# Kernel tuning notes

Hardware: AMD Instinct MI355X
Metric: run time of the kernel (lower is better)

The kernel has to match this reference:

```python
import jax, jax.numpy as jnp
import numpy as np
from jax import lax

B_, L_ = 2, 512
D_MODEL, EXPAND, HEAD_DIM, NGROUPS, D_STATE, D_CONV = 512, 2, 64, 1, 64, 3
D_INNER = EXPAND * D_MODEL            # 1024
NHEADS = D_INNER // HEAD_DIM          # 16
CONV_DIM = D_INNER + 2 * NGROUPS * D_STATE   # 1152
D_IN_PROJ = 2 * D_INNER + 2 * NGROUPS * D_STATE + NHEADS  # 2192
RMS_EPS = 1e-5


def silu(x):
    return x * jax.nn.sigmoid(x)


def segsum(x):
    # x: (..., T) -> (..., T, T); out[..., i, j] = sum_{j<k<=i} x[..., k], -inf above diag
    T = x.shape[-1]
    xr = jnp.broadcast_to(x[..., None], x.shape + (T,))
    keep = jnp.tril(jnp.ones((T, T), dtype=bool), -1)
    xr = jnp.where(keep, xr, 0.0)
    s = jnp.cumsum(xr, axis=-2)
    diag = jnp.tril(jnp.ones((T, T), dtype=bool), 0)
    return jnp.where(diag, s, -jnp.inf)


def ssd(x, A, Bm, Cm, chunk):
    # x: (b,l,h,p), A: (b,l,h), Bm/Cm: (b,l,g,n); chunk==1 as in the source forward
    b, l, h, p = x.shape
    c = l // chunk
    n = Bm.shape[-1]
    x = x.reshape(b, c, chunk, h, p)
    Bm = Bm.reshape(b, c, chunk, Bm.shape[2], n)
    Cm = Cm.reshape(b, c, chunk, Cm.shape[2], n)
    A = A.reshape(b, c, chunk, h).transpose(0, 3, 1, 2)        # (b,h,c,l)
    A_cumsum = jnp.cumsum(A, axis=-1)
    Lmat = jnp.exp(segsum(A))                                   # (b,h,c,l,l)
    # broadcast group dim (g==1) to heads, matching torch.einsum broadcasting
    Bb = jnp.broadcast_to(Bm, (b, c, chunk, h, n))
    Cb = jnp.broadcast_to(Cm, (b, c, chunk, h, n))
    Y_diag = jnp.einsum('bclhn,bcshn,bhcls,bcshp->bclhp', Cb, Bb, Lmat, x)
    decay_states = jnp.exp(A_cumsum[:, :, :, -1:] - A_cumsum)   # (b,h,c,l)
    states = jnp.einsum('bclhn,bhcl,bclhp->bchpn', Bb, decay_states, x)
    states = jnp.concatenate([jnp.zeros_like(states[:, :1]), states], axis=1)  # (b,c+1,h,p,n)
    A_last = jnp.pad(A_cumsum[:, :, :, -1], ((0, 0), (0, 0), (1, 0)))          # (b,h,c+1)
    decay_chunk = jnp.exp(segsum(A_last))                       # (b,h,c+1,c+1)
    new_states = jnp.einsum('bhzc,bchpn->bzhpn', decay_chunk, states)
    states = new_states[:, :-1]                                 # (b,c,h,p,n)
    state_decay_out = jnp.exp(A_cumsum)
    Y_off = jnp.einsum('bclhn,bchpn,bhcl->bclhp', Cb, states, state_decay_out)
    return (Y_diag + Y_off).reshape(b, l, h, p)


def causal_dwconv(x, w, bias):
    # x: (B,L,C); w: (C,K) depthwise; torch pads (K-1) both sides then slices [:L] == left-pad only
    xt = x.transpose(0, 2, 1)
    y = lax.conv_general_dilated(xt, w[:, None, :], (1,), [(D_CONV - 1, 0)],
                                 feature_group_count=CONV_DIM,
                                 dimension_numbers=('NCH', 'OIH', 'NCH'))
    return y.transpose(0, 2, 1) + bias


def setup_inputs() -> dict:
    key = jax.random.key(0)
    ks = jax.random.split(key, 8)
    u = jax.random.normal(ks[0], (B_, L_, D_MODEL), dtype=jnp.float32)
    W_in = jax.random.normal(ks[1], (D_MODEL, D_IN_PROJ), dtype=jnp.float32) / np.sqrt(D_MODEL).astype(np.float32)
    conv_w = jax.random.normal(ks[2], (CONV_DIM, D_CONV), dtype=jnp.float32) * 0.3
    conv_b = jnp.zeros((CONV_DIM,), dtype=jnp.float32)
    dt = jnp.exp(jax.random.uniform(ks[3], (NHEADS,), dtype=jnp.float32)
                 * (np.float32(np.log(0.1)) - np.float32(np.log(0.001))) + np.float32(np.log(0.001)))
    dt = jnp.clip(dt, 1e-4, None)
    dt_bias = dt + jnp.log(-jnp.expm1(-dt))
    A_log = jnp.log(jax.random.uniform(ks[4], (NHEADS,), dtype=jnp.float32, minval=1.0, maxval=16.0))
    D_param = jnp.ones((NHEADS,), dtype=jnp.float32)
    rms_w = jnp.ones((D_INNER,), dtype=jnp.float32)
    W_out = jax.random.normal(ks[5], (D_INNER, D_MODEL), dtype=jnp.float32) / np.sqrt(D_INNER).astype(np.float32)
    return {"u": u, "W_in": W_in, "conv_w": conv_w, "conv_b": conv_b, "dt_bias": dt_bias,
            "A_log": A_log, "D_param": D_param, "rms_w": rms_w, "W_out": W_out}


def reference(u, W_in, conv_w, conv_b, dt_bias, A_log, D_param, rms_w, W_out):
    b, l, _ = u.shape
    zxbcdt = u @ W_in                                   # (b,l,D_IN_PROJ)
    z = zxbcdt[..., :D_INNER]
    xBC = zxbcdt[..., D_INNER:D_INNER + CONV_DIM]
    dt = zxbcdt[..., D_INNER + CONV_DIM:]
    dt = jax.nn.softplus(dt + dt_bias)                  # (b,l,h)
    A = -jnp.exp(A_log)                                 # (h,)
    xBC = silu(causal_dwconv(xBC, conv_w, conv_b))      # (b,l,CONV_DIM)
    x = xBC[..., :D_INNER].reshape(b, l, NHEADS, HEAD_DIM)
    Bm = xBC[..., D_INNER:D_INNER + D_STATE][:, :, None, :]     # (b,l,1,n)
    Cm = xBC[..., D_INNER + D_STATE:][:, :, None, :]            # (b,l,1,n)
    y = ssd(x * dt[..., None], A * dt, Bm, Cm, 1)       # (b,l,h,p)
    y = y + x * D_param[:, None]
    y = y.reshape(b, l, D_INNER)
    # gated RMSNorm
    yz = y * silu(z)
    y = yz * lax.rsqrt(jnp.mean(yz * yz, axis=-1, keepdims=True) + RMS_EPS) * rms_w
    return y @ W_out
```

## Files before the change

### kernel.cpp

```cpp
#include <hip/hip_runtime.h>
#include <hip/hip_bf16.h>

#define B_SZ 2
#define L_SZ 512
#define D_MODEL 512
#define D_INNER 1024
#define HEAD_DIM 64
#define NHEADS 16
#define D_STATE 64
#define D_CONV 3
#define CONV_DIM 1152
#define D_IN_PROJ 2192
#define BL (B_SZ * L_SZ)
#define RMS_EPS 1e-5f
#define QC 64
#define NCH 8
#define NPAD1 2304
#define PB 72

typedef __attribute__((ext_vector_type(8))) short short8t;
typedef __attribute__((ext_vector_type(8))) unsigned short ushort8t;
typedef __attribute__((ext_vector_type(4))) unsigned short ushort4t;
typedef __attribute__((ext_vector_type(4))) float f32x4;

__device__ __forceinline__ unsigned short f2bf(float f) {
    unsigned u = __float_as_uint(f);
    u += 0x7fff + ((u >> 16) & 1);
    return (unsigned short)(u >> 16);
}
__device__ __forceinline__ float bf2f(unsigned short u) {
    return __uint_as_float(((unsigned)u) << 16);
}

__device__ __forceinline__ void gload_lds16(const void* g, void* lds) {
    __builtin_amdgcn_global_load_lds(
        (const __attribute__((address_space(1))) unsigned int*)g,
        (__attribute__((address_space(3))) unsigned int*)lds, 16, 0, 0);
}

__device__ __forceinline__ void transpose_tile_bf16(const float* __restrict__ src,
                                                    unsigned short* __restrict__ dst,
                                                    int K, int Nin, int tile, int ntn) {
    __shared__ float T[64][65];
    int tid = threadIdx.x;
    int nt = tile % ntn, kt = tile / ntn;
    int n0 = nt * 64, k0 = kt * 64;
#pragma unroll
    for (int rr = 0; rr < 4; ++rr) {
        int k = k0 + (tid >> 4) + rr * 16;
        int nn = (tid & 15) * 4;
#pragma unroll
        for (int q = 0; q < 4; ++q) {
            int n = n0 + nn + q;
            T[(tid >> 4) + rr * 16][nn + q] = (n < Nin) ? src[(size_t)k * Nin + n] : 0.f;
        }
    }
    __syncthreads();
    int nn2 = tid >> 2, kc = tid & 3;
    unsigned short ov[16];
#pragma unroll
    for (int j = 0; j < 16; ++j) ov[j] = f2bf(T[kc * 16 + j][nn2]);
    unsigned short* p = dst + (size_t)(n0 + nn2) * K + k0 + kc * 16;
    *(ushort8t*)p = *(ushort8t*)&ov[0];
    *(ushort8t*)(p + 8) = *(ushort8t*)&ov[8];
}

__global__ __launch_bounds__(256) void prep_kernel(const float* __restrict__ W_in,
                                                   const float* __restrict__ W_out,
                                                   const float* __restrict__ u,
                                                   unsigned short* __restrict__ Wt1,
                                                   unsigned short* __restrict__ Wt2,
                                                   unsigned short* __restrict__ u_bf) {
    int bid = blockIdx.x;
    if (bid < 288) {
        transpose_tile_bf16(W_in, Wt1, D_MODEL, D_IN_PROJ, bid, 36);
    } else if (bid < 416) {
        transpose_tile_bf16(W_out, Wt2, D_INNER, D_MODEL, bid - 288, 8);
    } else {
        int i = ((bid - 416) * 256 + threadIdx.x) * 8;
        float4 v0 = *(const float4*)(u + i);
        float4 v1 = *(const float4*)(u + i + 4);
        unsigned short ov[8] = {f2bf(v0.x), f2bf(v0.y), f2bf(v0.z), f2bf(v0.w),
                                f2bf(v1.x), f2bf(v1.y), f2bf(v1.z), f2bf(v1.w)};
        *(ushort8t*)(u_bf + i) = *(ushort8t*)&ov[0];
    }
}

__global__ __launch_bounds__(256) void gemm_mfma64(const unsigned short* __restrict__ A,
                                                   const unsigned short* __restrict__ Bt,
                                                   float* __restrict__ C,
                                                   int N, int K) {
    __shared__ char sm[49152];
    int tid = threadIdx.x;
    int w = tid >> 6, l = tid & 63;
    int m0 = blockIdx.y * 64, n0 = blockIdx.x * 64;
    int wm = w >> 1, wn = w & 1;

    f32x4 acc[2][2];
#pragma unroll
    for (int i = 0; i < 2; ++i)
#pragma unroll
        for (int j = 0; j < 2; ++j) acc[i][j] = (f32x4){0.f, 0.f, 0.f, 0.f};

    auto stage = [&](const unsigned short* src, int row0, int k0, char* dst) {
#pragma unroll
        for (int p = 0; p < 2; ++p) {
            int c = w * 2 + p;
            int row = c * 8 + (l >> 3);
            int scb = ((l & 7) << 4) ^ ((row & 7) << 4);
            gload_lds16(src + (size_t)(row0 + row) * K + k0 + (scb >> 1), dst + c * 1024);
        }
    };

    int nkt = K / 64;
    stage(A, m0, 0, sm);
    stage(Bt, n0, 0, sm + 8192);
    if (nkt > 1) {
        stage(A, m0, 64, sm + 16384);
        stage(Bt, n0, 64, sm + 16384 + 8192);
    }

    for (int kt = 0; kt < nkt; ++kt) {
        if (kt + 2 < nkt) {
            char* d = sm + ((kt + 2) % 3) * 16384;
            stage(A, m0, (kt + 2) * 64, d);
            stage(Bt, n0, (kt + 2) * 64, d + 8192);
        }
        int inflight = nkt - 1 - kt;
        if (inflight >= 2)      asm volatile("s_waitcnt vmcnt(8)" ::: "memory");
        else if (inflight == 1) asm volatile("s_waitcnt vmcnt(4)" ::: "memory");
        else                    asm volatile("s_waitcnt vmcnt(0)" ::: "memory");
        __builtin_amdgcn_s_barrier();

        const char* Ab = sm + (kt % 3) * 16384;
        const char* Bb = Ab + 8192;
#pragma unroll
        for (int kk = 0; kk < 2; ++kk) {
            short8t af[2], bf[2];
#pragma unroll
            for (int i = 0; i < 2; ++i) {
                int r = wm * 32 + i * 16 + (l & 15);
                int cb = (kk * 64 + (l >> 4) * 16) ^ ((r & 7) << 4);
                af[i] = *(const short8t*)(Ab + r * 128 + cb);
            }
#pragma unroll
            for (int j = 0; j < 2; ++j) {
                int r = wn * 32 + j * 16 + (l & 15);
                int cb = (kk * 64 + (l >> 4) * 16) ^ ((r & 7) << 4);
                bf[j] = *(const short8t*)(Bb + r * 128 + cb);
            }
#pragma unroll
            for (int i = 0; i < 2; ++i)
#pragma unroll
                for (int j = 0; j < 2; ++j)
                    acc[i][j] = __builtin_amdgcn_mfma_f32_16x16x32_bf16(af[i], bf[j], acc[i][j], 0, 0, 0);
        }
        __builtin_amdgcn_s_barrier();
    }

#pragma unroll
    for (int i = 0; i < 2; ++i)
#pragma unroll
        for (int j = 0; j < 2; ++j) {
            int row = m0 + wm * 32 + i * 16 + (l >> 4) * 4;
            int col = n0 + wn * 32 + j * 16 + (l & 15);
            if (col < N) {
#pragma unroll
                for (int r = 0; r < 4; ++r)
                    C[(size_t)(row + r) * N + col] = acc[i][j][r];
            }
        }
}

__device__ __forceinline__ float4 conv4(const float* __restrict__ prow, int gl, int zxcol,
                                        const float* __restrict__ conv_w,
                                        const float* __restrict__ conv_b) {
    float4 v2 = *(const float4*)(prow + zxcol);
    float4 v1 = make_float4(0.f, 0.f, 0.f, 0.f), v0 = v1;
    if (gl >= 1) v1 = *(const float4*)(prow - D_IN_PROJ + zxcol);
    if (gl >= 2) v0 = *(const float4*)(prow - 2 * D_IN_PROJ + zxcol);
    int ch = zxcol - D_INNER;
    float4 o;
    float a;
    a = conv_b[ch+0] + conv_w[(ch+0)*3]*v0.x + conv_w[(ch+0)*3+1]*v1.x + conv_w[(ch+0)*3+2]*v2.x;
    o.x = a / (1.f + __expf(-a));
    a = conv_b[ch+1] + conv_w[(ch+1)*3]*v0.y + conv_w[(ch+1)*3+1]*v1.y + conv_w[(ch+1)*3+2]*v2.y;
    o.y = a / (1.f + __expf(-a));
    a = conv_b[ch+2] + conv_w[(ch+2)*3]*v0.z + conv_w[(ch+2)*3+1]*v1.z + conv_w[(ch+2)*3+2]*v2.z;
    o.z = a / (1.f + __expf(-a));
    a = conv_b[ch+3] + conv_w[(ch+3)*3]*v0.w + conv_w[(ch+3)*3+1]*v1.w + conv_w[(ch+3)*3+2]*v2.w;
    o.w = a / (1.f + __expf(-a));
    return o;
}

__global__ __launch_bounds__(256) void ssd_passA(const float* __restrict__ zxbcdt,
                                                 const float* __restrict__ conv_w,
                                                 const float* __restrict__ conv_b,
                                                 const float* __restrict__ dt_bias,
                                                 const float* __restrict__ A_log,
                                                 const float* __restrict__ D_param,
                                                 float* __restrict__ y,
                                                 float* __restrict__ Zbuf,
                                                 float* __restrict__ Ebuf) {
    int blk = blockIdx.x;
    int h = blk & 15;
    int c = (blk >> 4) & 7;
    int b = blk >> 7;
    int tid = threadIdx.x;

    __shared__ __align__(16) unsigned short Cs_bf[QC][PB];
    __shared__ __align__(16) unsigned short Bs_bf[QC][PB];
    __shared__ __align__(16) unsigned short BT_bf[QC][PB];
    __shared__ __align__(16) unsigned short XDT_bf[QC][PB];
    __shared__ __align__(16) unsigned short XDTw_bf[QC][PB];
    __shared__ __align__(16) unsigned short P_bf[QC][PB];
    __shared__ float csh[QC], dts[QC], wh[QC];

    int bl0 = b * L_SZ + c * QC;
    const float* zb = zxbcdt + (size_t)bl0 * D_IN_PROJ;

    if (tid < 64) {
        int t = tid;
        float draw = zb[(size_t)t * D_IN_PROJ + 2 * D_INNER + 2 * D_STATE + h];
        float dtv = draw + dt_bias[h];
        dtv = (dtv > 20.f) ? dtv : log1pf(expf(dtv));
        float A = -expf(A_log[h]);
        float cs = A * dtv;
#pragma unroll
        for (int off = 1; off < 64; off <<= 1) {
            float tmp = __shfl_up(cs, off);
            if (t >= off) cs += tmp;
        }
        float cs63 = __shfl(cs, 63);
        dts[t] = dtv;
        csh[t] = cs;
        wh[t] = __expf(cs63 - cs);
        Ebuf[(((size_t)(b * NHEADS + h) * NCH) + c) * QC + t] = __expf(cs);
    }

    int row16 = tid >> 4;
    int col4 = (tid & 15) * 4;
#pragma unroll
    for (int r = 0; r < 4; ++r) {
        int t = r * 16 + row16;
        int gl = c * QC + t;
        const float* prow = zb + (size_t)t * D_IN_PROJ;
        float4 Bv = conv4(prow, gl, D_INNER + D_INNER + col4, conv_w, conv_b);
        float4 Cv = conv4(prow, gl, D_INNER + D_INNER + D_STATE + col4, conv_w, conv_b);
        ushort4t bq = {f2bf(Bv.x), f2bf(Bv.y), f2bf(Bv.z), f2bf(Bv.w)};
        ushort4t cq = {f2bf(Cv.x), f2bf(Cv.y), f2bf(Cv.z), f2bf(Cv.w)};
        *(ushort4t*)&Bs_bf[t][col4] = bq;
        *(ushort4t*)&Cs_bf[t][col4] = cq;
#pragma unroll
        for (int q = 0; q < 4; ++q) BT_bf[col4 + q][t] = bq[q];
    }
    __syncthreads();

#pragma unroll
    for (int r = 0; r < 4; ++r) {
        int t = r * 16 + row16;
        int gl = c * QC + t;
        const float* prow = zb + (size_t)t * D_IN_PROJ;
        float4 xv = conv4(prow, gl, D_INNER + h * HEAD_DIM + col4, conv_w, conv_b);
        float d = dts[t], wt = wh[t];
        xv.x *= d; xv.y *= d; xv.z *= d; xv.w *= d;
        ushort4t xq = {f2bf(xv.x), f2bf(xv.y), f2bf(xv.z), f2bf(xv.w)};
        ushort4t xwq = {f2bf(xv.x * wt), f2bf(xv.y * wt), f2bf(xv.z * wt), f2bf(xv.w * wt)};
#pragma unroll
        for (int q = 0; q < 4; ++q) {
            XDT_bf[col4 + q][t] = xq[q];
            XDTw_bf[col4 + q][t] = xwq[q];
        }
    }

    int l = tid & 63, wv = tid >> 6;
    int wm = wv >> 1, wn = wv & 1;
    int fr = l & 15, fq = l >> 4;

    {
        f32x4 g[2][2];
#pragma unroll
        for (int i = 0; i < 2; ++i)
#pragma unroll
            for (int j = 0; j < 2; ++j) g[i][j] = (f32x4){0.f, 0.f, 0.f, 0.f};
#pragma unroll
        for (int kk = 0; kk < 2; ++kk) {
            short8t af[2], bb[2];
#pragma unroll
            for (int i = 0; i < 2; ++i)
                af[i] = *(const short8t*)&Cs_bf[wm * 32 + i * 16 + fr][kk * 32 + fq * 8];
#pragma unroll
            for (int j = 0; j < 2; ++j)
                bb[j] = *(const short8t*)&Bs_bf[wn * 32 + j * 16 + fr][kk * 32 + fq * 8];
#pragma unroll
            for (int i = 0; i < 2; ++i)
#pragma unroll
                for (int j = 0; j < 2; ++j)
                    g[i][j] = __builtin_amdgcn_mfma_f32_16x16x32_bf16(af[i], bb[j], g[i][j], 0, 0, 0);
        }
#pragma unroll
        for (int i = 0; i < 2; ++i)
#pragma unroll
            for (int j = 0; j < 2; ++j) {
                int s = wn * 32 + j * 16 + fr;
                float css = csh[s];
#pragma unroll
                for (int r = 0; r < 4; ++r) {
                    int t = wm * 32 + i * 16 + fq * 4 + r;
                    float v = (s <= t) ? g[i][j][r] * __expf(csh[t] - css) : 0.f;
                    P_bf[t][s] = f2bf(v);
                }
            }
    }
    __syncthreads();

    {
        f32x4 yv[2][2];
#pragma unroll
        for (int i = 0; i < 2; ++i)
#pragma unroll
            for (int j = 0; j < 2; ++j) yv[i][j] = (f32x4){0.f, 0.f, 0.f, 0.f};
#pragma unroll
        for (int kk = 0; kk < 2; ++kk) {
            short8t af[2], bb[2];
#pragma unroll
            for (int i = 0; i < 2; ++i)
                af[i] = *(const short8t*)&P_bf[wm * 32 + i * 16 + fr][kk * 32 + fq * 8];
#pragma unroll
            for (int j = 0; j < 2; ++j)
                bb[j] = *(const short8t*)&XDT_bf[wn * 32 + j * 16 + fr][kk * 32 + fq * 8];
#pragma unroll
            for (int i = 0; i < 2; ++i)
#pragma unroll
                for (int j = 0; j < 2; ++j)
                    yv[i][j] = __builtin_amdgcn_mfma_f32_16x16x32_bf16(af[i], bb[j], yv[i][j], 0, 0, 0);
        }
        float Dp = D_param[h];
#pragma unroll
        for (int i = 0; i < 2; ++i)
#pragma unroll
            for (int j = 0; j < 2; ++j) {
                int p = wn * 32 + j * 16 + fr;
#pragma unroll
                for (int r = 0; r < 4; ++r) {
                    int t = wm * 32 + i * 16 + fq * 4 + r;
                    float xval = bf2f(XDT_bf[p][t]);
                    float fct = Dp / dts[t];
                    y[(size_t)(bl0 + t) * D_INNER + h * HEAD_DIM + p] =
                        yv[i][j][r] + fct * xval;
                }
            }
    }

    {
        f32x4 zv[2][2];
#pragma unroll
        for (int i = 0; i < 2; ++i)
#pragma unroll
            for (int j = 0; j < 2; ++j) zv[i][j] = (f32x4){0.f, 0.f, 0.f, 0.f};
#pragma unroll
        for (int kk = 0; kk < 2; ++kk) {
            short8t af[2], bb[2];
#pragma unroll
            for (int i = 0; i < 2; ++i)
                af[i] = *(const short8t*)&XDTw_bf[wm * 32 + i * 16 + fr][kk * 32 + fq * 8];
#pragma unroll
            for (int j = 0; j < 2; ++j)
                bb[j] = *(const short8t*)&BT_bf[wn * 32 + j * 16 + fr][kk * 32 + fq * 8];
#pragma unroll
            for (int i = 0; i < 2; ++i)
#pragma unroll
                for (int j = 0; j < 2; ++j)
                    zv[i][j] = __builtin_amdgcn_mfma_f32_16x16x32_bf16(af[i], bb[j], zv[i][j], 0, 0, 0);
        }
        float* Zr = Zbuf + (((size_t)(b * NHEADS + h) * NCH) + c) * (HEAD_DIM * D_STATE);
#pragma unroll
        for (int i = 0; i < 2; ++i)
#pragma unroll
            for (int j = 0; j < 2; ++j) {
                int n = wn * 32 + j * 16 + fr;
#pragma unroll
                for (int r = 0; r < 4; ++r) {
                    int p = wm * 32 + i * 16 + fq * 4 + r;
                    Zr[p * D_STATE + n] = zv[i][j][r];
                }
            }
    }
}

__global__ __launch_bounds__(256) void ssd_passC(const float* __restrict__ zxbcdt,
                                                 const float* __restrict__ conv_w,
                                                 const float* __restrict__ conv_b,
                                                 const float* __restrict__ Zbuf,
                                                 const float* __restrict__ Ebuf,
                                                 float* __restrict__ y) {
    int blk = blockIdx.x;
    int h = blk & 15;
    int c = (blk >> 4) & 7;
    int b = blk >> 7;
    if (c == 0) return;
    int tid = threadIdx.x;

    __shared__ __align__(16) unsigned short Cs_bf[QC][PB];
    __shared__ __align__(16) unsigned short S_bf[QC][PB];
    __shared__ float Eh[QC];

    int bl0 = b * L_SZ + c * QC;
    const float* zb = zxbcdt + (size_t)bl0 * D_IN_PROJ;
    const float* Zb = Zbuf + ((size_t)(b * NHEADS + h) * NCH) * (HEAD_DIM * D_STATE);
    const float* Eb = Ebuf + ((size_t)(b * NHEADS + h) * NCH) * QC;

    {
        int p = tid >> 2, nq = (tid & 3) * 16;
        float S16[16];
#pragma unroll
        for (int q = 0; q < 16; ++q) S16[q] = 0.f;
        float wgt = 1.f;
        for (int j = c - 1; j >= 0; --j) {
            const float* Zj = Zb + (size_t)j * (HEAD_DIM * D_STATE) + p * D_STATE + nq;
#pragma unroll
            for (int q4 = 0; q4 < 4; ++q4) {
                float4 z = *(const float4*)(Zj + q4 * 4);
                S16[q4 * 4 + 0] += wgt * z.x;
                S16[q4 * 4 + 1] += wgt * z.y;
                S16[q4 * 4 + 2] += wgt * z.z;
                S16[q4 * 4 + 3] += wgt * z.w;
            }
            wgt *= Eb[(size_t)j * QC + 63];
        }
#pragma unroll
        for (int q4 = 0; q4 < 4; ++q4) {
            ushort4t s4 = {f2bf(S16[q4 * 4 + 0]), f2bf(S16[q4 * 4 + 1]),
                           f2bf(S16[q4 * 4 + 2]), f2bf(S16[q4 * 4 + 3])};
            *(ushort4t*)&S_bf[p][nq + q4 * 4] = s4;
        }
    }

    int row16 = tid >> 4, col4 = (tid & 15) * 4;
#pragma unroll
    for (int r = 0; r < 4; ++r) {
        int t = r * 16 + row16;
        int gl = c * QC + t;
        float4 Cv = conv4(zb + (size_t)t * D_IN_PROJ, gl,
                          D_INNER + D_INNER + D_STATE + col4, conv_w, conv_b);
        ushort4t cq = {f2bf(Cv.x), f2bf(Cv.y), f2bf(Cv.z), f2bf(Cv.w)};
        *(ushort4t*)&Cs_bf[t][col4] = cq;
    }
    if (tid < 64)
        Eh[tid] = Ebuf[(((size_t)(b * NHEADS + h) * NCH) + c) * QC + tid];
    __syncthreads();

    int l = tid & 63, wv = tid >> 6;
    int wm = wv >> 1, wn = wv & 1;
    int fr = l & 15, fq = l >> 4;
    f32x4 acc[2][2];
#pragma unroll
    for (int i = 0; i < 2; ++i)
#pragma unroll
        for (int j = 0; j < 2; ++j) acc[i][j] = (f32x4){0.f, 0.f, 0.f, 0.f};
#pragma unroll
    for (int kk = 0; kk < 2; ++kk) {
        short8t af[2], bb[2];
#pragma unroll
        for (int i = 0; i < 2; ++i)
            af[i] = *(const short8t*)&Cs_bf[wm * 32 + i * 16 + fr][kk * 32 + fq * 8];
#pragma unroll
        for (int j = 0; j < 2; ++j)
            bb[j] = *(const short8t*)&S_bf[wn * 32 + j * 16 + fr][kk * 32 + fq * 8];
#pragma unroll
        for (int i = 0; i < 2; ++i)
#pragma unroll
            for (int j = 0; j < 2; ++j)
                acc[i][j] = __builtin_amdgcn_mfma_f32_16x16x32_bf16(af[i], bb[j], acc[i][j], 0, 0, 0);
    }
#pragma unroll
    for (int i = 0; i < 2; ++i)
#pragma unroll
        for (int j = 0; j < 2; ++j) {
            int p = wn * 32 + j * 16 + fr;
#pragma unroll
            for (int r = 0; r < 4; ++r) {
                int t = wm * 32 + i * 16 + fq * 4 + r;
                float* yp = y + (size_t)(bl0 + t) * D_INNER + h * HEAD_DIM + p;
                *yp += Eh[t] * acc[i][j][r];
            }
        }
}

__global__ __launch_bounds__(256) void gated_rmsnorm_kernel(const float* __restrict__ zxbcdt,
                                                            const float* __restrict__ y,
                                                            const float* __restrict__ rms_w,
                                                            unsigned short* __restrict__ yn_bf) {
    int bl = blockIdx.x;
    int tid = threadIdx.x;
    __shared__ float red[4];
    __shared__ float sscale;
    float vals[4];
    float sumsq = 0.f;
#pragma unroll
    for (int i = 0; i < 4; ++i) {
        int col = tid + i * 256;
        float yv = y[(size_t)bl * D_INNER + col];
        float z = zxbcdt[(size_t)bl * D_IN_PROJ + col];
        float yz = yv * (z / (1.f + expf(-z)));
        vals[i] = yz;
        sumsq += yz * yz;
    }
#pragma unroll
    for (int off = 32; off; off >>= 1) sumsq += __shfl_xor(sumsq, off);
    int wave = tid >> 6, lane = tid & 63;
    if (lane == 0) red[wave] = sumsq;
    __syncthreads();
    if (tid == 0) {
        float t = red[0] + red[1] + red[2] + red[3];
        sscale = rsqrtf(t / (float)D_INNER + RMS_EPS);
    }
    __syncthreads();
    float sc = sscale;
#pragma unroll
    for (int i = 0; i < 4; ++i) {
        int col = tid + i * 256;
        yn_bf[(size_t)bl * D_INNER + col] = f2bf(vals[i] * sc * rms_w[col]);
    }
}

extern "C" void kernel_launch(void* const* d_in, const int* in_sizes, int n_in,
                              void* d_out, int out_size, void* d_ws, size_t ws_size,
                              hipStream_t stream) {
    const float* u       = (const float*)d_in[0];
    const float* W_in    = (const float*)d_in[1];
    const float* conv_w  = (const float*)d_in[2];
    const float* conv_b  = (const float*)d_in[3];
    const float* dt_bias = (const float*)d_in[4];
    const float* A_log   = (const float*)d_in[5];
    const float* D_param = (const float*)d_in[6];
    const float* rms_w   = (const float*)d_in[7];
    const float* W_out   = (const float*)d_in[8];
    float* out = (float*)d_out;

    float* ws = (float*)d_ws;
    float* zxbcdt = ws;
    float* y      = zxbcdt + (size_t)BL * D_IN_PROJ;
    float* Zbuf   = y + (size_t)BL * D_INNER;
    float* Ebuf   = Zbuf + (size_t)32 * NCH * 4096;
    unsigned short* u_bf  = (unsigned short*)(Ebuf + 32 * NCH * QC);
    unsigned short* Wt1   = u_bf + (size_t)BL * D_MODEL;
    unsigned short* Wt2   = Wt1 + (size_t)NPAD1 * D_MODEL;
    unsigned short* yn_bf = Wt2 + (size_t)D_MODEL * D_INNER;

    prep_kernel<<<672, 256, 0, stream>>>(W_in, W_out, u, Wt1, Wt2, u_bf);

    gemm_mfma64<<<dim3(NPAD1 / 64, BL / 64), 256, 0, stream>>>(
        u_bf, Wt1, zxbcdt, D_IN_PROJ, D_MODEL);

    ssd_passA<<<B_SZ * NCH * NHEADS, 256, 0, stream>>>(
        zxbcdt, conv_w, conv_b, dt_bias, A_log, D_param, y, Zbuf, Ebuf);
    ssd_passC<<<B_SZ * NCH * NHEADS, 256, 0, stream>>>(
        zxbcdt, conv_w, conv_b, Zbuf, Ebuf, y);

    gated_rmsnorm_kernel<<<BL, 256, 0, stream>>>(zxbcdt, y, rms_w, yn_bf);

    gemm_mfma64<<<dim3(D_MODEL / 64, BL / 64), 256, 0, stream>>>(
        yn_bf, Wt2, out, D_MODEL, D_INNER);
}
```

Before: 47.46 us.

## Fuse gated RMSNorm into output GEMM and fold rms weight into W_out

Removes the separate gated RMSNorm kernel and its bf16 intermediate. The output GEMM now loads y and z, applies the SiLU gate and converts to bf16 as it stages A tiles, and accumulates per-row sums of squares so the rsqrt scale is applied in the epilogue. rms_w is folded into the transposed W_out during prep, and passC no longer launches idle blocks for chunk 0. This saves one launch and a full round trip through memory. The cost is that each of the 8 column blocks recomputes the gate and row norms, and the GEMM uses smaller 32-row tiles.

```diff
diff --git a/kernel.cpp b/kernel.cpp
--- a/kernel.cpp
+++ b/kernel.cpp
@@ -39,6 +39,7 @@
 }
 
 __device__ __forceinline__ void transpose_tile_bf16(const float* __restrict__ src,
+                                                    const float* __restrict__ scale,
                                                     unsigned short* __restrict__ dst,
                                                     int K, int Nin, int tile, int ntn) {
     __shared__ float T[64][65];
@@ -48,11 +49,12 @@
 #pragma unroll
     for (int rr = 0; rr < 4; ++rr) {
         int k = k0 + (tid >> 4) + rr * 16;
+        float sc = scale ? scale[k] : 1.f;
         int nn = (tid & 15) * 4;
 #pragma unroll
         for (int q = 0; q < 4; ++q) {
             int n = n0 + nn + q;
-            T[(tid >> 4) + rr * 16][nn + q] = (n < Nin) ? src[(size_t)k * Nin + n] : 0.f;
+            T[(tid >> 4) + rr * 16][nn + q] = (n < Nin) ? src[(size_t)k * Nin + n] * sc : 0.f;
         }
     }
     __syncthreads();
@@ -67,15 +69,16 @@
 
 __global__ __launch_bounds__(256) void prep_kernel(const float* __restrict__ W_in,
                                                    const float* __restrict__ W_out,
+                                                   const float* __restrict__ rms_w,
                                                    const float* __restrict__ u,
                                                    unsigned short* __restrict__ Wt1,
                                                    unsigned short* __restrict__ Wt2,
                                                    unsigned short* __restrict__ u_bf) {
     int bid = blockIdx.x;
     if (bid < 288) {
-        transpose_tile_bf16(W_in, Wt1, D_MODEL, D_IN_PROJ, bid, 36);
+        transpose_tile_bf16(W_in, nullptr, Wt1, D_MODEL, D_IN_PROJ, bid, 36);
     } else if (bid < 416) {
-        transpose_tile_bf16(W_out, Wt2, D_INNER, D_MODEL, bid - 288, 8);
+        transpose_tile_bf16(W_out, rms_w, Wt2, D_INNER, D_MODEL, bid - 288, 8);
     } else {
         int i = ((bid - 416) * 256 + threadIdx.x) * 8;
         float4 v0 = *(const float4*)(u + i);
@@ -396,9 +399,9 @@
                                                  float* __restrict__ y) {
     int blk = blockIdx.x;
     int h = blk & 15;
-    int c = (blk >> 4) & 7;
-    int b = blk >> 7;
-    if (c == 0) return;
+    int q = blk >> 4;
+    int c = 1 + (q % 7);
+    int b = q / 7;
     int tid = threadIdx.x;
 
     __shared__ __align__(16) unsigned short Cs_bf[QC][PB];
@@ -414,7 +417,7 @@
         int p = tid >> 2, nq = (tid & 3) * 16;
         float S16[16];
 #pragma unroll
-        for (int q = 0; q < 16; ++q) S16[q] = 0.f;
+        for (int qq = 0; qq < 16; ++qq) S16[qq] = 0.f;
         float wgt = 1.f;
         for (int j = c - 1; j >= 0; --j) {
             const float* Zj = Zb + (size_t)j * (HEAD_DIM * D_STATE) + p * D_STATE + nq;
@@ -487,40 +490,117 @@
         }
 }
 
-__global__ __launch_bounds__(256) void gated_rmsnorm_kernel(const float* __restrict__ zxbcdt,
-                                                            const float* __restrict__ y,
-                                                            const float* __restrict__ rms_w,
-                                                            unsigned short* __restrict__ yn_bf) {
-    int bl = blockIdx.x;
+__global__ __launch_bounds__(256) void gemm_out_fused(const float* __restrict__ y,
+                                                      const float* __restrict__ zxbcdt,
+                                                      const unsigned short* __restrict__ Bt,
+                                                      float* __restrict__ out) {
+    __shared__ char sm[2][12288];
+    __shared__ float red[32][8];
+    __shared__ float srow[32];
     int tid = threadIdx.x;
-    __shared__ float red[4];
-    __shared__ float sscale;
-    float vals[4];
+    int w = tid >> 6, l = tid & 63;
+    int m0 = blockIdx.y * 32, n0 = blockIdx.x * 64;
+    int wm = w >> 1, wn = w & 1;
+
+    f32x4 acc[2];
+    acc[0] = (f32x4){0.f, 0.f, 0.f, 0.f};
+    acc[1] = (f32x4){0.f, 0.f, 0.f, 0.f};
+
+    int ar = tid >> 3, ac8 = tid & 7;
+    const float* yrow = y + (size_t)(m0 + ar) * D_INNER + ac8 * 8;
+    const float* zrow = zxbcdt + (size_t)(m0 + ar) * D_IN_PROJ + ac8 * 8;
     float sumsq = 0.f;
-#pragma unroll
-    for (int i = 0; i < 4; ++i) {
-        int col = tid + i * 256;
-        float yv = y[(size_t)bl * D_INNER + col];
-        float z = zxbcdt[(size_t)bl * D_IN_PROJ + col];
-        float yz = yv * (z / (1.f + expf(-z)));
-        vals[i] = yz;
-        sumsq += yz * yz;
-    }
-#pragma unroll
-    for (int off = 32; off; off >>= 1) sumsq += __shfl_xor(sumsq, off);
-    int wave = tid >> 6, lane = tid & 63;
-    if (lane == 0) red[wave] = sumsq;
+
+    auto stageB = [&](int k0, char* dstB) {
+#pragma unroll
+        for (int p = 0; p < 2; ++p) {
+            int cc = w * 2 + p;
+            int row = cc * 8 + (l >> 3);
+            int scb = ((l & 7) << 4) ^ ((row & 7) << 4);
+            gload_lds16(Bt + (size_t)(n0 + row) * D_INNER + k0 + (scb >> 1), dstB + cc * 1024);
+        }
+    };
+
+    float4 vy0, vy1, vz0, vz1;
+    auto loadA = [&](int k0) {
+        vy0 = *(const float4*)(yrow + k0);
+        vy1 = *(const float4*)(yrow + k0 + 4);
+        vz0 = *(const float4*)(zrow + k0);
+        vz1 = *(const float4*)(zrow + k0 + 4);
+    };
+    auto writeA = [&](char* dstA) {
+        float yv[8] = {vy0.x, vy0.y, vy0.z, vy0.w, vy1.x, vy1.y, vy1.z, vy1.w};
+        float zv[8] = {vz0.x, vz0.y, vz0.z, vz0.w, vz1.x, vz1.y, vz1.z, vz1.w};
+        unsigned short o[8];
+#pragma unroll
+        for (int qq = 0; qq < 8; ++qq) {
+            float vv = yv[qq] * (zv[qq] / (1.f + __expf(-zv[qq])));
+            sumsq += vv * vv;
+            o[qq] = f2bf(vv);
+        }
+        int b0 = ac8 * 16;
+        *(ushort8t*)(dstA + ar * 128 + (b0 ^ ((ar & 7) << 4))) = *(ushort8t*)o;
+    };
+
+    loadA(0);
+    stageB(0, sm[0] + 4096);
+    writeA(sm[0]);
+    asm volatile("s_waitcnt lgkmcnt(0)" ::: "memory");
+
+    for (int kt = 0; kt < 16; ++kt) {
+        int cur = kt & 1;
+        if (kt + 1 < 16) {
+            loadA((kt + 1) * 64);
+            stageB((kt + 1) * 64, sm[cur ^ 1] + 4096);
+            asm volatile("s_waitcnt vmcnt(6)" ::: "memory");
+        } else {
+            asm volatile("s_waitcnt vmcnt(0)" ::: "memory");
+        }
+        __builtin_amdgcn_s_barrier();
+
+        const char* Ab = sm[cur];
+        const char* Bb = sm[cur] + 4096;
+#pragma unroll
+        for (int kk = 0; kk < 2; ++kk) {
+            short8t af;
+            {
+                int r = wm * 16 + (l & 15);
+                int cb = (kk * 64 + (l >> 4) * 16) ^ ((r & 7) << 4);
+                af = *(const short8t*)(Ab + r * 128 + cb);
+            }
+#pragma unroll
+            for (int j = 0; j < 2; ++j) {
+                int r = wn * 32 + j * 16 + (l & 15);
+                int cb = (kk * 64 + (l >> 4) * 16) ^ ((r & 7) << 4);
+                short8t bfv = *(const short8t*)(Bb + r * 128 + cb);
+                acc[j] = __builtin_amdgcn_mfma_f32_16x16x32_bf16(af, bfv, acc[j], 0, 0, 0);
+            }
+        }
+        if (kt + 1 < 16) {
+            asm volatile("s_waitcnt vmcnt(2)" ::: "memory");
+            writeA((char*)sm[cur ^ 1]);
+            asm volatile("s_waitcnt lgkmcnt(0)" ::: "memory");
+        }
+        __builtin_amdgcn_s_barrier();
+    }
+
+    red[ar][ac8] = sumsq;
     __syncthreads();
-    if (tid == 0) {
-        float t = red[0] + red[1] + red[2] + red[3];
-        sscale = rsqrtf(t / (float)D_INNER + RMS_EPS);
+    if (tid < 32) {
+        float s = 0.f;
+#pragma unroll
+        for (int qq = 0; qq < 8; ++qq) s += red[tid][qq];
+        srow[tid] = rsqrtf(s / (float)D_INNER + RMS_EPS);
     }
     __syncthreads();
-    float sc = sscale;
-#pragma unroll
-    for (int i = 0; i < 4; ++i) {
-        int col = tid + i * 256;
-        yn_bf[(size_t)bl * D_INNER + col] = f2bf(vals[i] * sc * rms_w[col]);
+
+#pragma unroll
+    for (int j = 0; j < 2; ++j) {
+        int col = n0 + wn * 32 + j * 16 + (l & 15);
+        int rl = wm * 16 + (l >> 4) * 4;
+#pragma unroll
+        for (int r = 0; r < 4; ++r)
+            out[(size_t)(m0 + rl + r) * D_MODEL + col] = acc[j][r] * srow[rl + r];
     }
 }
 
@@ -546,20 +626,17 @@
     unsigned short* u_bf  = (unsigned short*)(Ebuf + 32 * NCH * QC);
     unsigned short* Wt1   = u_bf + (size_t)BL * D_MODEL;
     unsigned short* Wt2   = Wt1 + (size_t)NPAD1 * D_MODEL;
-    unsigned short* yn_bf = Wt2 + (size_t)D_MODEL * D_INNER;
-
-    prep_kernel<<<672, 256, 0, stream>>>(W_in, W_out, u, Wt1, Wt2, u_bf);
+
+    prep_kernel<<<672, 256, 0, stream>>>(W_in, W_out, rms_w, u, Wt1, Wt2, u_bf);
 
     gemm_mfma64<<<dim3(NPAD1 / 64, BL / 64), 256, 0, stream>>>(
         u_bf, Wt1, zxbcdt, D_IN_PROJ, D_MODEL);
 
     ssd_passA<<<B_SZ * NCH * NHEADS, 256, 0, stream>>>(
         zxbcdt, conv_w, conv_b, dt_bias, A_log, D_param, y, Zbuf, Ebuf);
-    ssd_passC<<<B_SZ * NCH * NHEADS, 256, 0, stream>>>(
+    ssd_passC<<<224, 256, 0, stream>>>(
         zxbcdt, conv_w, conv_b, Zbuf, Ebuf, y);
 
-    gated_rmsnorm_kernel<<<BL, 256, 0, stream>>>(zxbcdt, y, rms_w, yn_bf);
-
-    gemm_mfma64<<<dim3(D_MODEL / 64, BL / 64), 256, 0, stream>>>(
-        yn_bf, Wt2, out, D_MODEL, D_INNER);
-}
+    gemm_out_fused<<<dim3(D_MODEL / 64, BL / 32), 256, 0, stream>>>(
+        y, zxbcdt, Wt2, out);
+}
```

Result: slower. 61.34 us (+29.3%).
